# Optimization experiments

Measured on AMD Instinct MI355X. Metric: run time of the kernel, lower is better.

Reference implementation:

```python
import jax, jax.numpy as jnp
import numpy as np

H = 1024
L = 2

def setup_inputs() -> dict:
    key = jax.random.key(0)
    k1, k2, k3, k4, k5 = jax.random.split(key, 5)
    B, S = 32, 2048
    scale = 1.0 / np.sqrt(H)
    return {
        "query": jax.random.normal(k1, (B, 1, H * L), dtype=jnp.float32),
        "keys": jax.random.normal(k2, (B, S, H), dtype=jnp.float32),
        "Wa_w": jax.random.normal(k3, (H * L, H), dtype=jnp.float32) * scale,
        "Wa_b": jnp.zeros((H,), dtype=jnp.float32),
        "Ua_w": jax.random.normal(k4, (H, H), dtype=jnp.float32) * scale,
        "Ua_b": jnp.zeros((H,), dtype=jnp.float32),
        "Va_w": jax.random.normal(k5, (H, 1), dtype=jnp.float32) * scale,
        "Va_b": jnp.zeros((1,), dtype=jnp.float32),
    }

def reference(query, keys, Wa_w, Wa_b, Ua_w, Ua_b, Va_w, Va_b):
    # query: [B,1,H*L], keys: [B,S,H]
    q = jnp.einsum('bqd,dh->bqh', query, Wa_w) + Wa_b   # [B,1,H]
    k = jnp.einsum('bsd,dh->bsh', keys, Ua_w) + Ua_b    # [B,S,H]
    e = jnp.tanh(q + k)                                  # [B,S,H]
    scores = jnp.einsum('bsh,ho->bso', e, Va_w) + Va_b   # [B,S,1]
    scores = scores[:, :, 0][:, None, :]                 # [B,1,S]
    weights = jax.nn.softmax(scores, axis=-1)            # [B,1,S]
    context = jnp.einsum('bqs,bsh->bqh', weights, keys)  # [B,1,H]
    return (context, weights)
```

## Files before the change

kernel.cpp:

```cpp
#include <hip/hip_runtime.h>
#include <hip/hip_bf16.h>


typedef __attribute__((ext_vector_type(8))) short short8;
typedef __attribute__((ext_vector_type(4))) float floatx4;

__device__ __forceinline__ unsigned short f2bf(float f) {
    union { float f; unsigned int u; } c; c.f = f;
    unsigned int u = c.u + 0x7fffu + ((c.u >> 16) & 1u);
    return (unsigned short)(u >> 16);
}

__global__ __launch_bounds__(256) void qproj_k(
    const float* __restrict__ query, const float* __restrict__ Wa,
    const float* __restrict__ Wab, const float* __restrict__ Uab,
    float* __restrict__ qws)
{
    __shared__ float qs[2048];
    __shared__ float red[4][64];
    const int tid = threadIdx.x;
    const int b = blockIdx.x, hc = blockIdx.y;
    #pragma unroll
    for (int i = 0; i < 8; i++) qs[tid + 256*i] = query[b*2048 + tid + 256*i];
    __syncthreads();
    const int h_l = tid & 63, dg = tid >> 6;
    const int h = hc*64 + h_l;
    float acc = 0.f;
    const float* wp = Wa + (size_t)(dg*512)*1024 + h;
    const float* qp = qs + dg*512;
    #pragma unroll 4
    for (int d = 0; d < 512; d++) acc += qp[d] * wp[(size_t)d*1024];
    red[dg][h_l] = acc;
    __syncthreads();
    if (tid < 64) {
        float r = red[0][tid] + red[1][tid] + red[2][tid] + red[3][tid];
        int hh = hc*64 + tid;
        qws[b*1024 + hh] = r + Wab[hh] + Uab[hh];
    }
}

__global__ __launch_bounds__(256) void uat_k(const float* __restrict__ Ua,
                                             unsigned short* __restrict__ uat)
{
    __shared__ unsigned short t[64][65];
    const int x = threadIdx.x & 63, yy = threadIdx.x >> 6;
    const int d0 = blockIdx.x*64, h0 = blockIdx.y*64;
    #pragma unroll
    for (int i = 0; i < 16; i++) {
        int y = yy*16 + i;
        t[y][x] = f2bf(Ua[(size_t)(d0+y)*1024 + h0 + x]);
    }
    __syncthreads();
    #pragma unroll
    for (int i = 0; i < 16; i++) {
        int y = yy*16 + i;
        uat[(size_t)(h0+y)*1024 + d0 + x] = t[x][y];
    }
}

__global__ __launch_bounds__(256) void score_gemm(
    const float* __restrict__ keys,
    const unsigned short* __restrict__ uat,
    const float* __restrict__ qws,
    const float* __restrict__ Va,
    float* __restrict__ partial)
{
    __shared__ unsigned short aS[128][40];
    __shared__ unsigned short bS[128][40];
    const int tid = threadIdx.x;
    const int b = blockIdx.z;
    const int s0 = blockIdx.x * 128;
    const int h0 = blockIdx.y * 128;
    const int lane = tid & 63, wave = tid >> 6;
    const int quad = lane >> 4, l15 = lane & 15;
    const int wm = (wave & 1) * 64, wn = (wave >> 1) * 64;

    floatx4 acc[4][4];
    #pragma unroll
    for (int i = 0; i < 4; i++)
        #pragma unroll
        for (int j = 0; j < 4; j++) acc[i][j] = (floatx4)0.0f;

    const float4* keys4 = reinterpret_cast<const float4*>(keys) + (size_t)(b*2048 + s0)*256;
    const uint4*  uat4  = reinterpret_cast<const uint4*>(uat) + (size_t)h0*128;

    for (int k0 = 0; k0 < 1024; k0 += 32) {
        #pragma unroll
        for (int i = 0; i < 4; i++) {
            int f = tid + 256*i;
            int row = f >> 3, c4 = f & 7;
            float4 v = keys4[(size_t)row*256 + (k0 >> 2) + c4];
            ushort4 o;
            o.x = f2bf(v.x); o.y = f2bf(v.y); o.z = f2bf(v.z); o.w = f2bf(v.w);
            *reinterpret_cast<ushort4*>(&aS[row][c4*4]) = o;
        }
        #pragma unroll
        for (int i = 0; i < 2; i++) {
            int f = tid + 256*i;
            int row = f >> 2, c8 = f & 3;
            uint4 v = uat4[(size_t)row*128 + (k0 >> 3) + c8];
            *reinterpret_cast<uint4*>(&bS[row][c8*8]) = v;
        }
        __syncthreads();
        short8 af[4], bf8[4];
        #pragma unroll
        for (int i = 0; i < 4; i++)
            af[i] = *reinterpret_cast<const short8*>(&aS[wm + 16*i + l15][quad*8]);
        #pragma unroll
        for (int j = 0; j < 4; j++)
            bf8[j] = *reinterpret_cast<const short8*>(&bS[wn + 16*j + l15][quad*8]);
        #pragma unroll
        for (int i = 0; i < 4; i++)
            #pragma unroll
            for (int j = 0; j < 4; j++)
                acc[i][j] = __builtin_amdgcn_mfma_f32_16x16x32_bf16(af[i], bf8[j], acc[i][j], 0, 0, 0);
        __syncthreads();
    }

    float qv[4], vav[4];
    #pragma unroll
    for (int j = 0; j < 4; j++) {
        int n = h0 + wn + 16*j + l15;
        qv[j]  = qws[b*1024 + n];
        vav[j] = Va[n];
    }
    const int slot = blockIdx.y * 2 + (wave >> 1);
    #pragma unroll
    for (int i = 0; i < 4; i++) {
        #pragma unroll
        for (int r = 0; r < 4; r++) {
            float p = 0.f;
            #pragma unroll
            for (int j = 0; j < 4; j++) {
                float x = qv[j] + acc[i][j][r];
                float e = __expf(2.f * x);
                float t = 1.f - 2.f * __builtin_amdgcn_rcpf(e + 1.f);
                p += vav[j] * t;
            }
            #pragma unroll
            for (int off = 1; off < 16; off <<= 1) p += __shfl_xor(p, off, 64);
            if (l15 == 0) {
                int m = wm + 16*i + quad*4 + r;
                partial[((size_t)b*16 + slot)*2048 + s0 + m] = p;
            }
        }
    }
}

__global__ __launch_bounds__(256) void softmax_k(const float* __restrict__ partial,
                                                 float* __restrict__ out_w)
{
    const int tid = threadIdx.x;
    const int b = blockIdx.x;
    __shared__ float wred[4], wred2[4];
    float sc[8];
    float mx = -3.0e38f;
    #pragma unroll
    for (int i = 0; i < 8; i++) {
        int s = tid + 256*i;
        float v = 0.f;
        #pragma unroll
        for (int ht = 0; ht < 16; ht++) v += partial[((size_t)b*16 + ht)*2048 + s];
        sc[i] = v; mx = fmaxf(mx, v);
    }
    #pragma unroll
    for (int off = 32; off >= 1; off >>= 1) mx = fmaxf(mx, __shfl_xor(mx, off, 64));
    if ((tid & 63) == 0) wred[tid >> 6] = mx;
    __syncthreads();
    mx = fmaxf(fmaxf(wred[0], wred[1]), fmaxf(wred[2], wred[3]));
    float e[8]; float lsum = 0.f;
    #pragma unroll
    for (int i = 0; i < 8; i++) { e[i] = __expf(sc[i] - mx); lsum += e[i]; }
    #pragma unroll
    for (int off = 32; off >= 1; off >>= 1) lsum += __shfl_xor(lsum, off, 64);
    if ((tid & 63) == 0) wred2[tid >> 6] = lsum;
    __syncthreads();
    float inv = 1.0f / (wred2[0] + wred2[1] + wred2[2] + wred2[3]);
    #pragma unroll
    for (int i = 0; i < 8; i++) out_w[b*2048 + tid + 256*i] = e[i] * inv;
}

__global__ __launch_bounds__(256) void ctx_k(const float* __restrict__ keys,
                                             const float* __restrict__ w,
                                             float* __restrict__ ctxp)
{
    const int tid = threadIdx.x;
    const int b = blockIdx.x, sc = blockIdx.y;
    const float4* k4 = reinterpret_cast<const float4*>(keys) + (size_t)(b*2048 + sc*256)*256;
    const float* wp = w + b*2048 + sc*256;
    float4 a; a.x = a.y = a.z = a.w = 0.f;
    #pragma unroll 4
    for (int s = 0; s < 256; s++) {
        float wv = wp[s];
        float4 kv = k4[(size_t)s*256 + tid];
        a.x += wv*kv.x; a.y += wv*kv.y; a.z += wv*kv.z; a.w += wv*kv.w;
    }
    reinterpret_cast<float4*>(ctxp)[((size_t)b*8 + sc)*256 + tid] = a;
}

__global__ __launch_bounds__(256) void ctxsum_k(const float* __restrict__ ctxp,
                                                float* __restrict__ out)
{
    const int idx = blockIdx.x*256 + threadIdx.x;
    const int b = idx >> 10, h = idx & 1023;
    float v = 0.f;
    #pragma unroll
    for (int sc = 0; sc < 8; sc++) v += ctxp[((size_t)b*8 + sc)*1024 + h];
    out[idx] = v;
}

extern "C" void kernel_launch(void* const* d_in, const int* in_sizes, int n_in,
                              void* d_out, int out_size, void* d_ws, size_t ws_size,
                              hipStream_t stream)
{
    const float* query = (const float*)d_in[0];
    const float* keys  = (const float*)d_in[1];
    const float* Wa_w  = (const float*)d_in[2];
    const float* Wa_b  = (const float*)d_in[3];
    const float* Ua_w  = (const float*)d_in[4];
    const float* Ua_b  = (const float*)d_in[5];
    const float* Va_w  = (const float*)d_in[6];

    char* ws = (char*)d_ws;
    float*          qws     = (float*)(ws);
    unsigned short* uat     = (unsigned short*)(ws + 131072);
    float*          partial = (float*)(ws + 131072 + 2097152);
    float*          ctxp    = (float*)(ws + 131072 + 2097152 + 4194304);

    float* out_ctx = (float*)d_out;
    float* out_w   = out_ctx + 32*1024;

    qproj_k  <<<dim3(32, 16),    256, 0, stream>>>(query, Wa_w, Wa_b, Ua_b, qws);
    uat_k    <<<dim3(16, 16),    256, 0, stream>>>(Ua_w, uat);
    score_gemm<<<dim3(16, 8, 32), 256, 0, stream>>>(keys, uat, qws, Va_w, partial);
    softmax_k<<<dim3(32),        256, 0, stream>>>(partial, out_w);
    ctx_k    <<<dim3(32, 8),     256, 0, stream>>>(keys, out_w, ctxp);
    ctxsum_k <<<dim3(128),       256, 0, stream>>>(ctxp, out_ctx);
}
```

Measured before the change: 689.2 us.

## Pre-convert keys to bf16 and stream GEMM tiles via global_load_lds with swizzle

Adds a kernel that converts the whole keys tensor to bf16 once, so the score GEMM no longer re-reads fp32 keys and converts them in every h-tile block. The new GEMM loads A and B tiles directly into LDS with global_load_lds and an XOR swizzle in place of padding, removing register staging. The context reduction is also split across twice as many chunks for more parallelism. This needs a 128MB workspace and an extra full pass over keys, and falls back to the old path when the workspace is too small.

```diff
diff --git a/kernel.cpp b/kernel.cpp
--- a/kernel.cpp
+++ b/kernel.cpp
@@ -4,11 +4,21 @@
 
 typedef __attribute__((ext_vector_type(8))) short short8;
 typedef __attribute__((ext_vector_type(4))) float floatx4;
+
+typedef const __attribute__((address_space(1))) unsigned int gu32;
+typedef __attribute__((address_space(3))) unsigned int lu32;
 
 __device__ __forceinline__ unsigned short f2bf(float f) {
     union { float f; unsigned int u; } c; c.f = f;
     unsigned int u = c.u + 0x7fffu + ((c.u >> 16) & 1u);
     return (unsigned short)(u >> 16);
+}
+
+__device__ __forceinline__ void gld16(const unsigned short* g, unsigned short* l) {
+    __builtin_amdgcn_global_load_lds(
+        (gu32*)(uintptr_t)g,
+        (lu32*)(unsigned int)(uintptr_t)l,
+        16, 0, 0);
 }
 
 __global__ __launch_bounds__(256) void qproj_k(
@@ -58,11 +68,109 @@
     }
 }
 
-__global__ __launch_bounds__(256) void score_gemm(
-    const float* __restrict__ keys,
+__global__ __launch_bounds__(256) void kb16_k(const float4* __restrict__ in,
+                                              ushort4* __restrict__ out)
+{
+    const int base = blockIdx.x*1024 + threadIdx.x;
+    #pragma unroll
+    for (int j = 0; j < 4; j++) {
+        float4 v = in[base + 256*j];
+        ushort4 o;
+        o.x = f2bf(v.x); o.y = f2bf(v.y); o.z = f2bf(v.z); o.w = f2bf(v.w);
+        out[base + 256*j] = o;
+    }
+}
+
+__global__ __launch_bounds__(256) void score_gemm_fast(
+    const unsigned short* __restrict__ kb,
     const unsigned short* __restrict__ uat,
     const float* __restrict__ qws,
     const float* __restrict__ Va,
+    float* __restrict__ partial)
+{
+    __shared__ unsigned short aS[128*32];
+    __shared__ unsigned short bS[128*32];
+    const int tid = threadIdx.x;
+    const int b = blockIdx.z;
+    const int s0 = blockIdx.x * 128;
+    const int h0 = blockIdx.y * 128;
+    const int lane = tid & 63, wave = tid >> 6;
+    const int quad = lane >> 4, l15 = lane & 15;
+    const int wm = (wave & 1) * 64, wn = (wave >> 1) * 64;
+
+    const int srow = lane >> 2;
+    const int schunk = (lane & 3) ^ ((srow >> 1) & 3);
+
+    floatx4 acc[4][4];
+    #pragma unroll
+    for (int i = 0; i < 4; i++)
+        #pragma unroll
+        for (int j = 0; j < 4; j++) acc[i][j] = (floatx4)0.0f;
+
+    const unsigned short* kbase = kb + (size_t)(b*2048 + s0)*1024;
+    const unsigned short* ubase = uat + (size_t)h0*1024;
+    const int c0 = wave*2, c1 = wave*2 + 1;
+    const size_t aoff0 = (size_t)(c0*16 + srow)*1024 + schunk*8;
+    const size_t aoff1 = (size_t)(c1*16 + srow)*1024 + schunk*8;
+
+    for (int k0 = 0; k0 < 1024; k0 += 32) {
+        gld16(kbase + aoff0 + k0, aS + c0*512);
+        gld16(kbase + aoff1 + k0, aS + c1*512);
+        gld16(ubase + aoff0 + k0, bS + c0*512);
+        gld16(ubase + aoff1 + k0, bS + c1*512);
+        __syncthreads();
+        short8 af[4], bf8[4];
+        #pragma unroll
+        for (int i = 0; i < 4; i++) {
+            int row = wm + 16*i + l15;
+            af[i] = *reinterpret_cast<const short8*>(aS + row*32 + ((quad ^ ((row>>1)&3)) * 8));
+        }
+        #pragma unroll
+        for (int j = 0; j < 4; j++) {
+            int row = wn + 16*j + l15;
+            bf8[j] = *reinterpret_cast<const short8*>(bS + row*32 + ((quad ^ ((row>>1)&3)) * 8));
+        }
+        #pragma unroll
+        for (int i = 0; i < 4; i++)
+            #pragma unroll
+            for (int j = 0; j < 4; j++)
+                acc[i][j] = __builtin_amdgcn_mfma_f32_16x16x32_bf16(af[i], bf8[j], acc[i][j], 0, 0, 0);
+        __syncthreads();
+    }
+
+    float qv[4], vav[4];
+    #pragma unroll
+    for (int j = 0; j < 4; j++) {
+        int n = h0 + wn + 16*j + l15;
+        qv[j]  = qws[b*1024 + n];
+        vav[j] = Va[n];
+    }
+    const int slot = blockIdx.y * 2 + (wave >> 1);
+    #pragma unroll
+    for (int i = 0; i < 4; i++) {
+        #pragma unroll
+        for (int r = 0; r < 4; r++) {
+            float p = 0.f;
+            #pragma unroll
+            for (int j = 0; j < 4; j++) {
+                float x = qv[j] + acc[i][j][r];
+                float e = __expf(2.f * x);
+                float t = 1.f - 2.f * __builtin_amdgcn_rcpf(e + 1.f);
+                p += vav[j] * t;
+            }
+            #pragma unroll
+            for (int off = 1; off < 16; off <<= 1) p += __shfl_xor(p, off, 64);
+            if (l15 == 0) {
+                int m = wm + 16*i + quad*4 + r;
+                partial[((size_t)b*16 + slot)*2048 + s0 + m] = p;
+            }
+        }
+    }
+}
+
+__global__ __launch_bounds__(256) void score_gemm(
+    const float* __restrict__ keys, const unsigned short* __restrict__ uat,
+    const float* __restrict__ qws, const float* __restrict__ Va,
     float* __restrict__ partial)
 {
     __shared__ unsigned short aS[128][40];
@@ -182,30 +290,29 @@
 
 __global__ __launch_bounds__(256) void ctx_k(const float* __restrict__ keys,
                                              const float* __restrict__ w,
-                                             float* __restrict__ ctxp)
+                                             float* __restrict__ ctxp, int sper)
 {
     const int tid = threadIdx.x;
     const int b = blockIdx.x, sc = blockIdx.y;
-    const float4* k4 = reinterpret_cast<const float4*>(keys) + (size_t)(b*2048 + sc*256)*256;
-    const float* wp = w + b*2048 + sc*256;
+    const float4* k4 = reinterpret_cast<const float4*>(keys) + (size_t)(b*2048 + sc*sper)*256;
+    const float* wp = w + b*2048 + sc*sper;
     float4 a; a.x = a.y = a.z = a.w = 0.f;
     #pragma unroll 4
-    for (int s = 0; s < 256; s++) {
+    for (int s = 0; s < sper; s++) {
         float wv = wp[s];
         float4 kv = k4[(size_t)s*256 + tid];
         a.x += wv*kv.x; a.y += wv*kv.y; a.z += wv*kv.z; a.w += wv*kv.w;
     }
-    reinterpret_cast<float4*>(ctxp)[((size_t)b*8 + sc)*256 + tid] = a;
+    reinterpret_cast<float4*>(ctxp)[((size_t)b*gridDim.y + sc)*256 + tid] = a;
 }
 
 __global__ __launch_bounds__(256) void ctxsum_k(const float* __restrict__ ctxp,
-                                                float* __restrict__ out)
+                                                float* __restrict__ out, int nc)
 {
     const int idx = blockIdx.x*256 + threadIdx.x;
     const int b = idx >> 10, h = idx & 1023;
     float v = 0.f;
-    #pragma unroll
-    for (int sc = 0; sc < 8; sc++) v += ctxp[((size_t)b*8 + sc)*1024 + h];
+    for (int s = 0; s < nc; s++) v += ctxp[((size_t)b*nc + s)*1024 + h];
     out[idx] = v;
 }
 
@@ -223,17 +330,28 @@
 
     char* ws = (char*)d_ws;
     float*          qws     = (float*)(ws);
-    unsigned short* uat     = (unsigned short*)(ws + 131072);
-    float*          partial = (float*)(ws + 131072 + 2097152);
-    float*          ctxp    = (float*)(ws + 131072 + 2097152 + 4194304);
+    unsigned short* uat     = (unsigned short*)(ws + (131072));
+    float*          partial = (float*)(ws + (131072 + 2097152));
+    float*          ctxp    = (float*)(ws + (131072 + 2097152 + 4194304));
+    unsigned short* kb      = (unsigned short*)(ws + (131072 + 2097152 + 4194304 + 2097152));
+    const size_t NEED_FAST = 131072ull + 2097152 + 4194304 + 2097152 + 134217728;
 
     float* out_ctx = (float*)d_out;
     float* out_w   = out_ctx + 32*1024;
 
-    qproj_k  <<<dim3(32, 16),    256, 0, stream>>>(query, Wa_w, Wa_b, Ua_b, qws);
-    uat_k    <<<dim3(16, 16),    256, 0, stream>>>(Ua_w, uat);
-    score_gemm<<<dim3(16, 8, 32), 256, 0, stream>>>(keys, uat, qws, Va_w, partial);
-    softmax_k<<<dim3(32),        256, 0, stream>>>(partial, out_w);
-    ctx_k    <<<dim3(32, 8),     256, 0, stream>>>(keys, out_w, ctxp);
-    ctxsum_k <<<dim3(128),       256, 0, stream>>>(ctxp, out_ctx);
-}
+    qproj_k <<<dim3(32, 16), 256, 0, stream>>>(query, Wa_w, Wa_b, Ua_b, qws);
+    uat_k   <<<dim3(16, 16), 256, 0, stream>>>(Ua_w, uat);
+
+    if (ws_size >= NEED_FAST) {
+        kb16_k         <<<dim3(16384),     256, 0, stream>>>((const float4*)keys, (ushort4*)kb);
+        score_gemm_fast<<<dim3(16, 8, 32), 256, 0, stream>>>(kb, uat, qws, Va_w, partial);
+        softmax_k      <<<dim3(32),        256, 0, stream>>>(partial, out_w);
+        ctx_k          <<<dim3(32, 16),    256, 0, stream>>>(keys, out_w, ctxp, 128);
+        ctxsum_k       <<<dim3(128),       256, 0, stream>>>(ctxp, out_ctx, 16);
+    } else {
+        score_gemm     <<<dim3(16, 8, 32), 256, 0, stream>>>(keys, uat, qws, Va_w, partial);
+        softmax_k      <<<dim3(32),        256, 0, stream>>>(partial, out_w);
+        ctx_k          <<<dim3(32, 8),     256, 0, stream>>>(keys, out_w, ctxp, 256);
+        ctxsum_k       <<<dim3(128),       256, 0, stream>>>(ctxp, out_ctx, 8);
+    }
+}
```

After: 677.7 us. Within noise of the previous version (-1.7%).
